# Kernel tuning notes

Measured on AMD Instinct MI355X. Metric: run time of the kernel, lower is better.

The kernel has to match this reference:

```python
import jax, jax.numpy as jnp
import numpy as np

D_MODEL = 1024
D_STATE = 16
D_CONV = 4
EXPAND = 2
D_INNER = EXPAND * D_MODEL          # 2048
DT_RANK = (D_MODEL + 15) // 16      # 64
BATCH = 2
SEQLEN = 2048


def setup_inputs() -> dict:
    key = jax.random.key(0)
    ks = jax.random.split(key, 10)

    def rn(k, shape, scale=0.02):
        return (jax.random.normal(k, shape, jnp.float32) * scale).astype(jnp.float32)

    x = jax.random.normal(ks[0], (BATCH, SEQLEN, D_MODEL), jnp.float32)
    W_in = rn(ks[1], (2 * D_INNER, D_MODEL))
    conv_w = rn(ks[2], (D_INNER, D_CONV), 0.1)
    conv_b = jnp.zeros((D_INNER,), jnp.float32)
    W_x = rn(ks[3], (DT_RANK + 2 * D_STATE, D_INNER))
    dt_std = DT_RANK ** -0.5
    W_dt = jax.random.uniform(ks[4], (D_INNER, DT_RANK), jnp.float32, -dt_std, dt_std)
    # dt bias init: inverse softplus of dt ~ LogUniform(1e-3, 1e-1)
    dt = jnp.exp(jax.random.uniform(ks[5], (D_INNER,), jnp.float32)
                 * (np.log(0.1) - np.log(0.001)) + np.log(0.001))
    dt = jnp.clip(dt, 1e-4, None)
    b_dt = dt + jnp.log(-jnp.expm1(-dt))
    # A_log = log(1..d_state) broadcast over d_inner (S4D-real init)
    A_log = jnp.log(jnp.tile(jnp.arange(1, D_STATE + 1, dtype=jnp.float32)[None, :],
                             (D_INNER, 1)))
    Dp = jnp.ones((D_INNER,), jnp.float32)
    W_out1 = rn(ks[6], (D_INNER, 2 * D_INNER))
    W_out2 = rn(ks[7], (D_MODEL, D_INNER))
    return {"x": x, "W_in": W_in, "conv_w": conv_w, "conv_b": conv_b,
            "W_x": W_x, "W_dt": W_dt, "b_dt": b_dt, "A_log": A_log,
            "Dp": Dp, "W_out1": W_out1, "W_out2": W_out2}


def _mefi_forward(x, W_in, conv_w, conv_b, W_x, W_dt, b_dt, A_log, Dp, W_out1, W_out2):
    B, L, _ = x.shape
    # in_proj: (b,l,d) -> (b, 2*d_inner, l)
    xz = jnp.einsum('bld,ed->bel', x, W_in)
    xi, z = xz[:, :D_INNER, :], xz[:, D_INNER:, :]

    # causal depthwise conv1d (left pad d_conv-1) + SiLU
    xc = jax.lax.conv_general_dilated(
        xi, conv_w[:, None, :], window_strides=(1,), padding=[(D_CONV - 1, 0)],
        dimension_numbers=('NCH', 'OIH', 'NCH'), feature_group_count=D_INNER)
    u = jax.nn.silu(xc + conv_b[None, :, None])  # (b, d_inner, l)

    # x_proj -> dt / B / C
    x_dbl = jnp.einsum('bdl,ed->ble', u, W_x)           # (b, l, dt_rank+2n)
    dt_r = x_dbl[..., :DT_RANK]                          # (b, l, r)
    Bm = x_dbl[..., DT_RANK:DT_RANK + D_STATE].transpose(0, 2, 1)  # (b, n, l)
    Cm = x_dbl[..., DT_RANK + D_STATE:].transpose(0, 2, 1)          # (b, n, l)
    dt = jnp.einsum('blr,dr->bdl', dt_r, W_dt)           # (b, d_inner, l)

    A = -jnp.exp(A_log)                                  # (d_inner, n)
    delta = jax.nn.softplus(dt + b_dt[None, :, None])    # (b, d_inner, l)

    # selective scan over time
    def step(s, inp):
        d_t, u_t, B_t, C_t = inp  # (b,d) (b,d) (b,n) (b,n)
        dA = jnp.exp(d_t[:, :, None] * A[None, :, :])
        s = dA * s + (d_t * u_t)[:, :, None] * B_t[:, None, :]
        y_t = jnp.einsum('bdn,bn->bd', s, C_t)
        return s, y_t

    s0 = jnp.zeros((B, D_INNER, D_STATE), delta.dtype)
    xs = (delta.transpose(2, 0, 1), u.transpose(2, 0, 1),
          Bm.transpose(2, 0, 1), Cm.transpose(2, 0, 1))
    _, ys = jax.lax.scan(step, s0, xs)                   # (l, b, d)
    y = ys.transpose(1, 2, 0)                            # (b, d, l)
    y = (y + Dp[None, :, None] * u) * jax.nn.silu(z)     # gated scan output

    # interaction term: tr_term = C^T @ S_t^T (S_t == A), plus D @ x
    y_t = jnp.einsum('bnl,dn->bld', Cm, A) \
        + jnp.einsum('d,bdl->bl', Dp, u)[..., None]      # (b, l, d_inner)

    # cat along channels then out_proj MLP
    y_cat = jnp.concatenate([y.transpose(0, 2, 1), y_t], axis=-1)  # (b, l, 2*d_inner)
    h = jnp.maximum(y_cat @ W_out1.T, 0.0)
    return h @ W_out2.T                                   # (b, l, d_model)


def reference(x, W_in, conv_w, conv_b, W_x, W_dt, b_dt, A_log, Dp, W_out1, W_out2):
    return _mefi_forward(x, W_in, conv_w, conv_b, W_x, W_dt, b_dt, A_log, Dp, W_out1, W_out2)
```

## Files before the change

### kernel.cpp

```cpp
#include <hip/hip_runtime.h>
#include <hip/hip_bf16.h>
#include <math.h>

#define D_MODEL 1024
#define D_STATE 16
#define D_INNER 2048
#define DT_RANK 64
#define BATCH   2
#define SEQLEN  2048
#define NPROJ   96
#define XSTR    128
#define NCHUNK  16
#define CHUNK   128
#define XKS     8

typedef __attribute__((ext_vector_type(8))) __bf16 bf16x8;
typedef __attribute__((ext_vector_type(4))) float f32x4;

__device__ __forceinline__ float silu_f(float x) { return x / (1.f + __expf(-x)); }

__device__ __forceinline__ void gload_lds16(const void* g, void* l) {
    __builtin_amdgcn_global_load_lds((const __attribute__((address_space(1))) void*)g,
                                     (__attribute__((address_space(3))) void*)l, 16, 0, 0);
}

template<int RELU, int OUT_BF16>
__global__ __launch_bounds__(256) void gemm_bf16_k(
    const __bf16* __restrict__ A, const __bf16* __restrict__ B, void* __restrict__ Cv,
    int K, int lda, int ldb, int ldc, long long sA, long long sB, long long sC)
{
    __shared__ alignas(16) __bf16 As[128 * 32];
    __shared__ alignas(16) __bf16 Bs[128 * 32];
    const int bz = blockIdx.z;
    A += (long long)bz * sA;
    B += (long long)bz * sB;
    int nwg = gridDim.x * gridDim.y;
    int flat = blockIdx.y * gridDim.x + blockIdx.x;
    int swz = (nwg & 7) ? flat : ((flat & 7) * (nwg >> 3) + (flat >> 3));
    const int m0 = (swz / gridDim.x) * 128, n0 = (swz % gridDim.x) * 128;
    const int tid = threadIdx.x;
    const int lane = tid & 63;
    const int wv = tid >> 6;
    const int wr = wv >> 1, wc = wv & 1;

    f32x4 acc[4][4];
    #pragma unroll
    for (int i = 0; i < 4; ++i)
        #pragma unroll
        for (int j = 0; j < 4; ++j) acc[i][j] = (f32x4){0.f, 0.f, 0.f, 0.f};

    const int ko = (lane >> 4) * 8;
    const int fr = lane & 15;

    for (int k0 = 0; k0 < K; k0 += 32) {
        #pragma unroll
        for (int q = 0; q < 2; ++q) {
            int f = tid + q * 256;
            int row = f >> 2, c16 = f & 3;
            gload_lds16(A + (long long)(m0 + row) * lda + k0 + c16 * 8, As + f * 8);
            gload_lds16(B + (long long)(n0 + row) * ldb + k0 + c16 * 8, Bs + f * 8);
        }
        __syncthreads();
        bf16x8 a[4], b[4];
        #pragma unroll
        for (int i = 0; i < 4; ++i) {
            a[i] = *(const bf16x8*)(As + (wr * 64 + i * 16 + fr) * 32 + ko);
            b[i] = *(const bf16x8*)(Bs + (wc * 64 + i * 16 + fr) * 32 + ko);
        }
        #pragma unroll
        for (int i = 0; i < 4; ++i)
            #pragma unroll
            for (int j = 0; j < 4; ++j)
                acc[i][j] = __builtin_amdgcn_mfma_f32_16x16x32_bf16(a[i], b[j], acc[i][j], 0, 0, 0);
        __syncthreads();
    }

    #pragma unroll
    for (int i = 0; i < 4; ++i) {
        const int row = m0 + wr * 64 + i * 16 + (lane >> 4) * 4;
        #pragma unroll
        for (int j = 0; j < 4; ++j) {
            const int col = n0 + wc * 64 + j * 16 + fr;
            #pragma unroll
            for (int r = 0; r < 4; ++r) {
                float v = acc[i][j][r];
                if (RELU) v = fmaxf(v, 0.f);
                if (OUT_BF16)
                    ((__bf16*)Cv)[(long long)bz * sC + (long long)(row + r) * ldc + col] = (__bf16)v;
                else
                    ((float*)Cv)[(long long)bz * sC + (long long)(row + r) * ldc + col] = v;
            }
        }
    }
}

__global__ void cvt_bf16_k(const float* __restrict__ in, __bf16* __restrict__ out, int n8) {
    int i = blockIdx.x * 256 + threadIdx.x;
    if (i >= n8) return;
    const f32x4* p = (const f32x4*)in + (long long)i * 2;
    f32x4 v0 = p[0], v1 = p[1];
    bf16x8 o;
    o[0] = (__bf16)v0[0]; o[1] = (__bf16)v0[1]; o[2] = (__bf16)v0[2]; o[3] = (__bf16)v0[3];
    o[4] = (__bf16)v1[0]; o[5] = (__bf16)v1[1]; o[6] = (__bf16)v1[2]; o[7] = (__bf16)v1[3];
    ((bf16x8*)out)[i] = o;
}

template<int SOFTPLUS>
__global__ __launch_bounds__(256) void gemm_nt_k(
    const float* __restrict__ A, const float* __restrict__ B, float* __restrict__ C,
    const float* __restrict__ bias,
    int M, int N, int K, int lda, int ldb, int ldc,
    long long sA, long long sB, long long sC)
{
    __shared__ float As[16][68];
    __shared__ float Bs[16][68];
    const int bz = blockIdx.z;
    A += (long long)bz * sA; B += (long long)bz * sB; C += (long long)bz * sC;
    const int m0 = blockIdx.y * 64, n0 = blockIdx.x * 64;
    const int tid = threadIdx.x;
    const int lk = tid & 15, lr = tid >> 4;
    const int tx = tid & 15, ty = tid >> 4;
    float acc[4][4] = {};
    for (int k0 = 0; k0 < K; k0 += 16) {
        #pragma unroll
        for (int q = 0; q < 4; ++q) {
            int i = lr + q * 16;
            As[lk][i] = A[(long long)(m0 + i) * lda + k0 + lk];
            Bs[lk][i] = B[(long long)(n0 + i) * ldb + k0 + lk];
        }
        __syncthreads();
        #pragma unroll
        for (int k = 0; k < 16; ++k) {
            float a[4], b[4];
            #pragma unroll
            for (int j = 0; j < 4; ++j) { a[j] = As[k][ty*4+j]; b[j] = Bs[k][tx*4+j]; }
            #pragma unroll
            for (int i = 0; i < 4; ++i)
                #pragma unroll
                for (int j = 0; j < 4; ++j) acc[i][j] += a[i] * b[j];
        }
        __syncthreads();
    }
    #pragma unroll
    for (int i = 0; i < 4; ++i) {
        const int m = m0 + ty * 4 + i;
        float bi = SOFTPLUS ? bias[m] : 0.f;
        #pragma unroll
        for (int j = 0; j < 4; ++j) {
            float v = acc[i][j];
            if (SOFTPLUS) {
                v += bi;
                v = fmaxf(v, 0.f) + log1pf(expf(-fabsf(v)));
            }
            C[(long long)m * ldc + n0 + tx*4 + j] = v;
        }
    }
}

__global__ void aneg_k(const float* __restrict__ A_log, float* __restrict__ Aneg) {
    int i = blockIdx.x * 256 + threadIdx.x;
    if (i < D_INNER * D_STATE) Aneg[i] = -expf(A_log[i]);
}

__global__ __launch_bounds__(256) void conv_silu_k(const float* __restrict__ xz,
    const float* __restrict__ cw, const float* __restrict__ cb,
    float* __restrict__ u, __bf16* __restrict__ ut)
{
    __shared__ float tile[32][33];
    const int b = blockIdx.z;
    const int d0 = blockIdx.y * 32, l0 = blockIdx.x * 32;
    const int lx = threadIdx.x, dy = threadIdx.y;
    #pragma unroll
    for (int j = 0; j < 4; ++j) {
        int d = d0 + dy + j * 8;
        const float* xi = xz + ((long long)b * 2 * D_INNER + d) * SEQLEN;
        int l = l0 + lx;
        float acc = cb[d];
        #pragma unroll
        for (int k = 0; k < 4; ++k) {
            int t = l + k - 3;
            if (t >= 0) acc += xi[t] * cw[d * 4 + k];
        }
        float v = silu_f(acc);
        u[((long long)b * D_INNER + d) * SEQLEN + l] = v;
        tile[dy + j * 8][lx] = v;
    }
    __syncthreads();
    #pragma unroll
    for (int j = 0; j < 4; ++j) {
        int l = l0 + dy + j * 8;
        ut[((long long)b * SEQLEN + l) * D_INNER + d0 + lx] = (__bf16)tile[lx][dy + j * 8];
    }
}

__global__ void xdbl_red_k(const float* __restrict__ xpart, float* __restrict__ xdbl) {
    int i = blockIdx.x * 256 + threadIdx.x;
    const f32x4* p = (const f32x4*)xpart;
    f32x4 s = p[i];
    #pragma unroll
    for (int ks = 1; ks < XKS; ++ks) {
        f32x4 v = p[(long long)ks * (BATCH * SEQLEN * XSTR / 4) + i];
        s.x += v.x; s.y += v.y; s.z += v.z; s.w += v.w;
    }
    ((f32x4*)xdbl)[i] = s;
}

__global__ __launch_bounds__(256) void scan_f_k(const float* __restrict__ delta,
    const float* __restrict__ u, const float* __restrict__ xdbl,
    const float* __restrict__ Aneg, float* __restrict__ y)
{
    __shared__ float combA[NCHUNK][16];
    __shared__ float combS[NCHUNK][16];
    __shared__ float sins[NCHUNK][16];
    __shared__ float lp[NCHUNK][16][17];
    const int tid = threadIdx.x;
    const int lane = tid & 63;
    const int n = lane & 15;
    const int c = (tid >> 6) * 4 + (lane >> 4);
    const int g = blockIdx.x;
    const int b = g >> 11, d = g & (D_INNER - 1);
    const float a = Aneg[d * D_STATE + n];
    const long long base = (long long)g * SEQLEN + c * CHUNK;
    const float4* dv = (const float4*)(delta + base);
    const float4* uv = (const float4*)(u + base);
    const float* xb = xdbl + ((long long)b * SEQLEN + c * CHUNK) * XSTR + DT_RANK + n;

    float4 pd[4], pu[4];
    float pB[16];
    #pragma unroll
    for (int i = 0; i < 4; ++i) { pd[i] = dv[i]; pu[i] = uv[i]; }
    #pragma unroll
    for (int i = 0; i < 16; ++i) pB[i] = xb[i * XSTR];

    float s = 0.f, ap = 1.f;
    for (int t0 = 0; t0 < CHUNK; t0 += 16) {
        float cd[16], cu[16], cB[16];
        #pragma unroll
        for (int i = 0; i < 4; ++i) {
            cd[4*i] = pd[i].x; cd[4*i+1] = pd[i].y; cd[4*i+2] = pd[i].z; cd[4*i+3] = pd[i].w;
            cu[4*i] = pu[i].x; cu[4*i+1] = pu[i].y; cu[4*i+2] = pu[i].z; cu[4*i+3] = pu[i].w;
        }
        #pragma unroll
        for (int i = 0; i < 16; ++i) cB[i] = pB[i];
        if (t0 + 16 < CHUNK) {
            const int nb = (t0 >> 2) + 4;
            #pragma unroll
            for (int i = 0; i < 4; ++i) { pd[i] = dv[nb + i]; pu[i] = uv[nb + i]; }
            const float* xn = xb + (t0 + 16) * XSTR;
            #pragma unroll
            for (int i = 0; i < 16; ++i) pB[i] = xn[i * XSTR];
        }
        float dA[16], wB[16];
        #pragma unroll
        for (int i = 0; i < 16; ++i) {
            dA[i] = __expf(cd[i] * a);
            wB[i] = cd[i] * cu[i] * cB[i];
        }
        #pragma unroll
        for (int i = 0; i < 16; ++i) {
            s = dA[i] * s + wB[i];
            ap *= dA[i];
        }
    }
    combA[c][n] = ap;
    combS[c][n] = s;
    __syncthreads();

    if (tid < 16) {
        float av[NCHUNK], sv[NCHUNK];
        #pragma unroll
        for (int cc = 0; cc < NCHUNK; ++cc) { av[cc] = combA[cc][tid]; sv[cc] = combS[cc][tid]; }
        float carry = 0.f;
        #pragma unroll
        for (int cc = 0; cc < NCHUNK; ++cc) {
            sins[cc][tid] = carry;
            carry = sv[cc] + av[cc] * carry;
        }
    }
    __syncthreads();

    float* yl = y + base;
    float pC[16];
    #pragma unroll
    for (int i = 0; i < 4; ++i) { pd[i] = dv[i]; pu[i] = uv[i]; }
    #pragma unroll
    for (int i = 0; i < 16; ++i) { pB[i] = xb[i * XSTR]; pC[i] = xb[i * XSTR + D_STATE]; }

    s = sins[c][n];
    for (int t0 = 0; t0 < CHUNK; t0 += 16) {
        float cd[16], cu[16], cB[16], cC[16];
        #pragma unroll
        for (int i = 0; i < 4; ++i) {
            cd[4*i] = pd[i].x; cd[4*i+1] = pd[i].y; cd[4*i+2] = pd[i].z; cd[4*i+3] = pd[i].w;
            cu[4*i] = pu[i].x; cu[4*i+1] = pu[i].y; cu[4*i+2] = pu[i].z; cu[4*i+3] = pu[i].w;
        }
        #pragma unroll
        for (int i = 0; i < 16; ++i) { cB[i] = pB[i]; cC[i] = pC[i]; }
        if (t0 + 16 < CHUNK) {
            const int nb = (t0 >> 2) + 4;
            #pragma unroll
            for (int i = 0; i < 4; ++i) { pd[i] = dv[nb + i]; pu[i] = uv[nb + i]; }
            const float* xn = xb + (t0 + 16) * XSTR;
            #pragma unroll
            for (int i = 0; i < 16; ++i) { pB[i] = xn[i * XSTR]; pC[i] = xn[i * XSTR + D_STATE]; }
        }
        float dA[16], wB[16];
        #pragma unroll
        for (int i = 0; i < 16; ++i) {
            dA[i] = __expf(cd[i] * a);
            wB[i] = cd[i] * cu[i] * cB[i];
        }
        #pragma unroll
        for (int i = 0; i < 16; ++i) {
            s = dA[i] * s + wB[i];
            lp[c][n][i] = s * cC[i];
        }
        float v[16];
        #pragma unroll
        for (int j = 0; j < 16; ++j) v[j] = lp[c][j][n];
        float acc = 0.f;
        #pragma unroll
        for (int j = 0; j < 16; ++j) acc += v[j];
        yl[t0 + n] = acc;
    }
}

__global__ void ssum_k(const float* __restrict__ u, const float* __restrict__ Dp,
                       float* __restrict__ S)
{
    int li = blockIdx.x * 256 + threadIdx.x;
    int c = blockIdx.y;
    int b = li >> 11, l = li & (SEQLEN - 1);
    const float* up = u + (long long)b * D_INNER * SEQLEN + l;
    float acc = 0.f;
    for (int d = c * 256; d < c * 256 + 256; ++d)
        acc += Dp[d] * up[(long long)d * SEQLEN];
    atomicAdd(&S[li], acc);
}

__global__ __launch_bounds__(256) void ytrans_k(const float* __restrict__ ysc,
    const float* __restrict__ u, const float* __restrict__ xz,
    const float* __restrict__ Dp, __bf16* __restrict__ ycat)
{
    __shared__ float tile[32][33];
    const int b = blockIdx.z;
    const int d0 = blockIdx.y * 32, l0 = blockIdx.x * 32;
    const int lx = threadIdx.x, dy = threadIdx.y;
    #pragma unroll
    for (int j = 0; j < 4; ++j) {
        int d = d0 + dy + j * 8;
        long long i  = ((long long)b * D_INNER + d) * SEQLEN + l0 + lx;
        long long iz = ((long long)b * 2 * D_INNER + D_INNER + d) * SEQLEN + l0 + lx;
        tile[dy + j * 8][lx] = (ysc[i] + Dp[d] * u[i]) * silu_f(xz[iz]);
    }
    __syncthreads();
    #pragma unroll
    for (int j = 0; j < 4; ++j) {
        int l = l0 + dy + j * 8;
        ycat[((long long)b * SEQLEN + l) * (2 * D_INNER) + d0 + lx] = (__bf16)tile[lx][dy + j * 8];
    }
}

__global__ __launch_bounds__(256) void yt_k(const float* __restrict__ xdbl,
    const float* __restrict__ Aneg, const float* __restrict__ S, __bf16* __restrict__ ycat)
{
    __shared__ float Cs[16][33];
    __shared__ float An[16][64];
    __shared__ float Sv[32];
    const int b = blockIdx.z;
    const int d0 = blockIdx.y * 64, l0 = blockIdx.x * 32;
    const int tid = threadIdx.x;
    for (int f = tid; f < 512; f += 256) {
        int n = f & 15, l = f >> 4;
        Cs[n][l] = xdbl[((long long)b * SEQLEN + l0 + l) * XSTR + DT_RANK + D_STATE + n];
    }
    for (int f = tid; f < 1024; f += 256) {
        int n = f & 15, d = f >> 4;
        An[n][d] = Aneg[(d0 + d) * D_STATE + n];
    }
    if (tid < 32) Sv[tid] = S[b * SEQLEN + l0 + tid];
    __syncthreads();
    const int dx = tid & 63, lg = tid >> 6;
    #pragma unroll
    for (int j = 0; j < 8; ++j) {
        int l = lg * 8 + j;
        float acc = Sv[l];
        #pragma unroll
        for (int n = 0; n < 16; ++n) acc += Cs[n][l] * An[n][dx];
        ycat[((long long)b * SEQLEN + l0 + l) * (2 * D_INNER) + D_INNER + d0 + dx] = (__bf16)acc;
    }
}

extern "C" void kernel_launch(void* const* d_in, const int* in_sizes, int n_in,
                              void* d_out, int out_size, void* d_ws, size_t ws_size,
                              hipStream_t stream)
{
    const float* x      = (const float*)d_in[0];
    const float* W_in   = (const float*)d_in[1];
    const float* conv_w = (const float*)d_in[2];
    const float* conv_b = (const float*)d_in[3];
    const float* W_x    = (const float*)d_in[4];
    const float* W_dt   = (const float*)d_in[5];
    const float* b_dt   = (const float*)d_in[6];
    const float* A_log  = (const float*)d_in[7];
    const float* Dp     = (const float*)d_in[8];
    const float* W_out1 = (const float*)d_in[9];
    const float* W_out2 = (const float*)d_in[10];
    float* out = (float*)d_out;
    float* ws  = (float*)d_ws;

    float* xz    = ws;
    float* u     = xz    + 16777216;
    float* xdblp = u     + 8388608;
    float* dtb   = xdblp + 524288;
    float* ysc   = dtb   + 8388608;
    float* Aneg  = ysc   + 8388608;
    float* S     = Aneg  + 32768;
    __bf16* ycat16 = (__bf16*)(S + 4096);
    __bf16* h16    = ycat16 + 16777216;
    __bf16* W_in16  = (__bf16*)u;
    __bf16* xb16    = W_in16 + 4194304;
    __bf16* Wout116 = (__bf16*)dtb;
    __bf16* Wout216 = Wout116 + 8388608;
    __bf16* ut16  = ycat16;
    __bf16* Wx16p = h16;
    float* xpart  = dtb;

    hipMemsetAsync(S, 0, 4096 * sizeof(float), stream);
    aneg_k<<<128, 256, 0, stream>>>(A_log, Aneg);

    cvt_bf16_k<<<2048, 256, 0, stream>>>(W_in, W_in16, 524288);
    cvt_bf16_k<<<2048, 256, 0, stream>>>(x, xb16, 524288);
    cvt_bf16_k<<<96, 256, 0, stream>>>(W_x, Wx16p, 24576);
    hipMemsetAsync(Wx16p + 96 * D_INNER, 0, 32 * D_INNER * sizeof(__bf16), stream);

    gemm_bf16_k<0, 0><<<dim3(16, 32, BATCH), 256, 0, stream>>>(
        W_in16, xb16, xz, D_MODEL, D_MODEL, D_MODEL, SEQLEN,
        0LL, (long long)SEQLEN * D_MODEL, (long long)4096 * SEQLEN);

    conv_silu_k<<<dim3(SEQLEN / 32, D_INNER / 32, BATCH), dim3(32, 8), 0, stream>>>(
        xz, conv_w, conv_b, u, ut16);

    gemm_bf16_k<0, 0><<<dim3(1, 32, XKS), 256, 0, stream>>>(
        ut16, Wx16p, xpart, D_INNER / XKS, D_INNER, D_INNER, XSTR,
        (long long)(D_INNER / XKS), (long long)(D_INNER / XKS),
        (long long)BATCH * SEQLEN * XSTR);
    xdbl_red_k<<<(BATCH * SEQLEN * XSTR / 4) / 256, 256, 0, stream>>>(xpart, xdblp);

    gemm_nt_k<1><<<dim3(SEQLEN / 64, D_INNER / 64, BATCH), 256, 0, stream>>>(
        W_dt, xdblp, dtb, b_dt, D_INNER, SEQLEN, DT_RANK, DT_RANK, XSTR, SEQLEN,
        0LL, (long long)SEQLEN * XSTR, (long long)D_INNER * SEQLEN);

    scan_f_k<<<BATCH * D_INNER, 256, 0, stream>>>(dtb, u, xdblp, Aneg, ysc);

    cvt_bf16_k<<<4096, 256, 0, stream>>>(W_out1, Wout116, 1048576);
    cvt_bf16_k<<<1024, 256, 0, stream>>>(W_out2, Wout216, 262144);

    ssum_k<<<dim3((BATCH * SEQLEN) / 256, 8), 256, 0, stream>>>(u, Dp, S);

    ytrans_k<<<dim3(SEQLEN / 32, D_INNER / 32, BATCH), dim3(32, 8), 0, stream>>>(ysc, u, xz, Dp, ycat16);

    yt_k<<<dim3(SEQLEN / 32, D_INNER / 64, BATCH), 256, 0, stream>>>(xdblp, Aneg, S, ycat16);

    gemm_bf16_k<1, 1><<<dim3(16, 32, 1), 256, 0, stream>>>(
        ycat16, Wout116, h16, 2 * D_INNER, 2 * D_INNER, 2 * D_INNER, D_INNER,
        0LL, 0LL, 0LL);

    gemm_bf16_k<0, 0><<<dim3(8, 32, 1), 256, 0, stream>>>(
        h16, Wout216, out, D_INNER, D_INNER, D_INNER, D_MODEL,
        0LL, 0LL, 0LL);
}
```

Measured before the change: 529.9 us.

## Store x_dbl transposed for coalesced scan loads and emit scan output in bf16

The x_proj GEMM now computes the transposed product, so x_dbl is stored as (feature, batch*seq). The scan kernel can then read B and C with contiguous float4 loads instead of strided scalar loads. The dt GEMM gains a transposed-B load path and yt_k is updated to match the new layout. The scan output is also written as bf16 to halve its write and read traffic, at some precision cost before the gating step.

```diff
diff --git a/kernel.cpp b/kernel.cpp
--- a/kernel.cpp
+++ b/kernel.cpp
@@ -10,6 +10,7 @@
 #define SEQLEN  2048
 #define NPROJ   96
 #define XSTR    128
+#define LFLAT   (BATCH * SEQLEN)
 #define NCHUNK  16
 #define CHUNK   128
 #define XKS     8
@@ -105,7 +106,7 @@
     ((bf16x8*)out)[i] = o;
 }
 
-template<int SOFTPLUS>
+template<int SOFTPLUS, int BT>
 __global__ __launch_bounds__(256) void gemm_nt_k(
     const float* __restrict__ A, const float* __restrict__ B, float* __restrict__ C,
     const float* __restrict__ bias,
@@ -126,7 +127,20 @@
         for (int q = 0; q < 4; ++q) {
             int i = lr + q * 16;
             As[lk][i] = A[(long long)(m0 + i) * lda + k0 + lk];
-            Bs[lk][i] = B[(long long)(n0 + i) * ldb + k0 + lk];
+        }
+        if (BT) {
+            #pragma unroll
+            for (int q = 0; q < 4; ++q) {
+                int row = (tid >> 6) + q * 4;
+                int col = tid & 63;
+                Bs[row][col] = B[(long long)(k0 + row) * ldb + n0 + col];
+            }
+        } else {
+            #pragma unroll
+            for (int q = 0; q < 4; ++q) {
+                int i = lr + q * 16;
+                Bs[lk][i] = B[(long long)(n0 + i) * ldb + k0 + lk];
+            }
         }
         __syncthreads();
         #pragma unroll
@@ -193,21 +207,21 @@
     }
 }
 
-__global__ void xdbl_red_k(const float* __restrict__ xpart, float* __restrict__ xdbl) {
+__global__ void xdbl_red_k(const float* __restrict__ xpart, float* __restrict__ xdT) {
     int i = blockIdx.x * 256 + threadIdx.x;
     const f32x4* p = (const f32x4*)xpart;
     f32x4 s = p[i];
     #pragma unroll
     for (int ks = 1; ks < XKS; ++ks) {
-        f32x4 v = p[(long long)ks * (BATCH * SEQLEN * XSTR / 4) + i];
+        f32x4 v = p[(long long)ks * (XSTR * LFLAT / 4) + i];
         s.x += v.x; s.y += v.y; s.z += v.z; s.w += v.w;
     }
-    ((f32x4*)xdbl)[i] = s;
+    ((f32x4*)xdT)[i] = s;
 }
 
 __global__ __launch_bounds__(256) void scan_f_k(const float* __restrict__ delta,
-    const float* __restrict__ u, const float* __restrict__ xdbl,
-    const float* __restrict__ Aneg, float* __restrict__ y)
+    const float* __restrict__ u, const float* __restrict__ xdT,
+    const float* __restrict__ Aneg, __bf16* __restrict__ y)
 {
     __shared__ float combA[NCHUNK][16];
     __shared__ float combS[NCHUNK][16];
@@ -223,14 +237,13 @@
     const long long base = (long long)g * SEQLEN + c * CHUNK;
     const float4* dv = (const float4*)(delta + base);
     const float4* uv = (const float4*)(u + base);
-    const float* xb = xdbl + ((long long)b * SEQLEN + c * CHUNK) * XSTR + DT_RANK + n;
-
-    float4 pd[4], pu[4];
-    float pB[16];
-    #pragma unroll
-    for (int i = 0; i < 4; ++i) { pd[i] = dv[i]; pu[i] = uv[i]; }
-    #pragma unroll
-    for (int i = 0; i < 16; ++i) pB[i] = xb[i * XSTR];
+    const long long lbase = (long long)b * SEQLEN + c * CHUNK;
+    const float4* bv = (const float4*)(xdT + (long long)(DT_RANK + n) * LFLAT + lbase);
+    const float4* cvv = (const float4*)(xdT + (long long)(DT_RANK + D_STATE + n) * LFLAT + lbase);
+
+    float4 pd[4], pu[4], pb[4];
+    #pragma unroll
+    for (int i = 0; i < 4; ++i) { pd[i] = dv[i]; pu[i] = uv[i]; pb[i] = bv[i]; }
 
     float s = 0.f, ap = 1.f;
     for (int t0 = 0; t0 < CHUNK; t0 += 16) {
@@ -239,16 +252,12 @@
         for (int i = 0; i < 4; ++i) {
             cd[4*i] = pd[i].x; cd[4*i+1] = pd[i].y; cd[4*i+2] = pd[i].z; cd[4*i+3] = pd[i].w;
             cu[4*i] = pu[i].x; cu[4*i+1] = pu[i].y; cu[4*i+2] = pu[i].z; cu[4*i+3] = pu[i].w;
-        }
-        #pragma unroll
-        for (int i = 0; i < 16; ++i) cB[i] = pB[i];
+            cB[4*i] = pb[i].x; cB[4*i+1] = pb[i].y; cB[4*i+2] = pb[i].z; cB[4*i+3] = pb[i].w;
+        }
         if (t0 + 16 < CHUNK) {
             const int nb = (t0 >> 2) + 4;
             #pragma unroll
-            for (int i = 0; i < 4; ++i) { pd[i] = dv[nb + i]; pu[i] = uv[nb + i]; }
-            const float* xn = xb + (t0 + 16) * XSTR;
-            #pragma unroll
-            for (int i = 0; i < 16; ++i) pB[i] = xn[i * XSTR];
+            for (int i = 0; i < 4; ++i) { pd[i] = dv[nb + i]; pu[i] = uv[nb + i]; pb[i] = bv[nb + i]; }
         }
         float dA[16], wB[16];
         #pragma unroll
@@ -279,12 +288,10 @@
     }
     __syncthreads();
 
-    float* yl = y + base;
-    float pC[16];
-    #pragma unroll
-    for (int i = 0; i < 4; ++i) { pd[i] = dv[i]; pu[i] = uv[i]; }
-    #pragma unroll
-    for (int i = 0; i < 16; ++i) { pB[i] = xb[i * XSTR]; pC[i] = xb[i * XSTR + D_STATE]; }
+    __bf16* yl = y + base;
+    float4 pc[4];
+    #pragma unroll
+    for (int i = 0; i < 4; ++i) { pd[i] = dv[i]; pu[i] = uv[i]; pb[i] = bv[i]; pc[i] = cvv[i]; }
 
     s = sins[c][n];
     for (int t0 = 0; t0 < CHUNK; t0 += 16) {
@@ -293,16 +300,16 @@
         for (int i = 0; i < 4; ++i) {
             cd[4*i] = pd[i].x; cd[4*i+1] = pd[i].y; cd[4*i+2] = pd[i].z; cd[4*i+3] = pd[i].w;
             cu[4*i] = pu[i].x; cu[4*i+1] = pu[i].y; cu[4*i+2] = pu[i].z; cu[4*i+3] = pu[i].w;
-        }
-        #pragma unroll
-        for (int i = 0; i < 16; ++i) { cB[i] = pB[i]; cC[i] = pC[i]; }
+            cB[4*i] = pb[i].x; cB[4*i+1] = pb[i].y; cB[4*i+2] = pb[i].z; cB[4*i+3] = pb[i].w;
+            cC[4*i] = pc[i].x; cC[4*i+1] = pc[i].y; cC[4*i+2] = pc[i].z; cC[4*i+3] = pc[i].w;
+        }
         if (t0 + 16 < CHUNK) {
             const int nb = (t0 >> 2) + 4;
             #pragma unroll
-            for (int i = 0; i < 4; ++i) { pd[i] = dv[nb + i]; pu[i] = uv[nb + i]; }
-            const float* xn = xb + (t0 + 16) * XSTR;
-            #pragma unroll
-            for (int i = 0; i < 16; ++i) { pB[i] = xn[i * XSTR]; pC[i] = xn[i * XSTR + D_STATE]; }
+            for (int i = 0; i < 4; ++i) {
+                pd[i] = dv[nb + i]; pu[i] = uv[nb + i];
+                pb[i] = bv[nb + i]; pc[i] = cvv[nb + i];
+            }
         }
         float dA[16], wB[16];
         #pragma unroll
@@ -321,7 +328,7 @@
         float acc = 0.f;
         #pragma unroll
         for (int j = 0; j < 16; ++j) acc += v[j];
-        yl[t0 + n] = acc;
+        yl[t0 + n] = (__bf16)acc;
     }
 }
 
@@ -338,7 +345,7 @@
     atomicAdd(&S[li], acc);
 }
 
-__global__ __launch_bounds__(256) void ytrans_k(const float* __restrict__ ysc,
+__global__ __launch_bounds__(256) void ytrans_k(const __bf16* __restrict__ ysc,
     const float* __restrict__ u, const float* __restrict__ xz,
     const float* __restrict__ Dp, __bf16* __restrict__ ycat)
 {
@@ -351,7 +358,7 @@
         int d = d0 + dy + j * 8;
         long long i  = ((long long)b * D_INNER + d) * SEQLEN + l0 + lx;
         long long iz = ((long long)b * 2 * D_INNER + D_INNER + d) * SEQLEN + l0 + lx;
-        tile[dy + j * 8][lx] = (ysc[i] + Dp[d] * u[i]) * silu_f(xz[iz]);
+        tile[dy + j * 8][lx] = ((float)ysc[i] + Dp[d] * u[i]) * silu_f(xz[iz]);
     }
     __syncthreads();
     #pragma unroll
@@ -361,7 +368,7 @@
     }
 }
 
-__global__ __launch_bounds__(256) void yt_k(const float* __restrict__ xdbl,
+__global__ __launch_bounds__(256) void yt_k(const float* __restrict__ xdT,
     const float* __restrict__ Aneg, const float* __restrict__ S, __bf16* __restrict__ ycat)
 {
     __shared__ float Cs[16][33];
@@ -371,8 +378,8 @@
     const int d0 = blockIdx.y * 64, l0 = blockIdx.x * 32;
     const int tid = threadIdx.x;
     for (int f = tid; f < 512; f += 256) {
-        int n = f & 15, l = f >> 4;
-        Cs[n][l] = xdbl[((long long)b * SEQLEN + l0 + l) * XSTR + DT_RANK + D_STATE + n];
+        int n = f >> 5, l = f & 31;
+        Cs[n][l] = xdT[(long long)(DT_RANK + D_STATE + n) * LFLAT + (long long)b * SEQLEN + l0 + l];
     }
     for (int f = tid; f < 1024; f += 256) {
         int n = f & 15, d = f >> 4;
@@ -411,12 +418,12 @@
 
     float* xz    = ws;
     float* u     = xz    + 16777216;
-    float* xdblp = u     + 8388608;
-    float* dtb   = xdblp + 524288;
-    float* ysc   = dtb   + 8388608;
-    float* Aneg  = ysc   + 8388608;
+    float* xdT   = u     + 8388608;
+    float* dtb   = xdT   + 524288;
+    float* Aneg  = dtb   + 8388608;
     float* S     = Aneg  + 32768;
-    __bf16* ycat16 = (__bf16*)(S + 4096);
+    __bf16* ysc16  = (__bf16*)(S + 4096);
+    __bf16* ycat16 = ysc16 + 8388608;
     __bf16* h16    = ycat16 + 16777216;
     __bf16* W_in16  = (__bf16*)u;
     __bf16* xb16    = W_in16 + 4194304;
@@ -441,26 +448,26 @@
     conv_silu_k<<<dim3(SEQLEN / 32, D_INNER / 32, BATCH), dim3(32, 8), 0, stream>>>(
         xz, conv_w, conv_b, u, ut16);
 
-    gemm_bf16_k<0, 0><<<dim3(1, 32, XKS), 256, 0, stream>>>(
-        ut16, Wx16p, xpart, D_INNER / XKS, D_INNER, D_INNER, XSTR,
+    gemm_bf16_k<0, 0><<<dim3(32, 1, XKS), 256, 0, stream>>>(
+        Wx16p, ut16, xpart, D_INNER / XKS, D_INNER, D_INNER, LFLAT,
         (long long)(D_INNER / XKS), (long long)(D_INNER / XKS),
-        (long long)BATCH * SEQLEN * XSTR);
-    xdbl_red_k<<<(BATCH * SEQLEN * XSTR / 4) / 256, 256, 0, stream>>>(xpart, xdblp);
-
-    gemm_nt_k<1><<<dim3(SEQLEN / 64, D_INNER / 64, BATCH), 256, 0, stream>>>(
-        W_dt, xdblp, dtb, b_dt, D_INNER, SEQLEN, DT_RANK, DT_RANK, XSTR, SEQLEN,
-        0LL, (long long)SEQLEN * XSTR, (long long)D_INNER * SEQLEN);
-
-    scan_f_k<<<BATCH * D_INNER, 256, 0, stream>>>(dtb, u, xdblp, Aneg, ysc);
+        (long long)XSTR * LFLAT);
+    xdbl_red_k<<<(XSTR * LFLAT / 4) / 256, 256, 0, stream>>>(xpart, xdT);
+
+    gemm_nt_k<1, 1><<<dim3(SEQLEN / 64, D_INNER / 64, BATCH), 256, 0, stream>>>(
+        W_dt, xdT, dtb, b_dt, D_INNER, SEQLEN, DT_RANK, DT_RANK, LFLAT, SEQLEN,
+        0LL, (long long)SEQLEN, (long long)D_INNER * SEQLEN);
+
+    scan_f_k<<<BATCH * D_INNER, 256, 0, stream>>>(dtb, u, xdT, Aneg, ysc16);
 
     cvt_bf16_k<<<4096, 256, 0, stream>>>(W_out1, Wout116, 1048576);
     cvt_bf16_k<<<1024, 256, 0, stream>>>(W_out2, Wout216, 262144);
 
     ssum_k<<<dim3((BATCH * SEQLEN) / 256, 8), 256, 0, stream>>>(u, Dp, S);
 
-    ytrans_k<<<dim3(SEQLEN / 32, D_INNER / 32, BATCH), dim3(32, 8), 0, stream>>>(ysc, u, xz, Dp, ycat16);
-
-    yt_k<<<dim3(SEQLEN / 32, D_INNER / 64, BATCH), 256, 0, stream>>>(xdblp, Aneg, S, ycat16);
+    ytrans_k<<<dim3(SEQLEN / 32, D_INNER / 32, BATCH), dim3(32, 8), 0, stream>>>(ysc16, u, xz, Dp, ycat16);
+
+    yt_k<<<dim3(SEQLEN / 32, D_INNER / 64, BATCH), 256, 0, stream>>>(xdT, Aneg, S, ycat16);
 
     gemm_bf16_k<1, 1><<<dim3(16, 32, 1), 256, 0, stream>>>(
         ycat16, Wout116, h16, 2 * D_INNER, 2 * D_INNER, 2 * D_INNER, D_INNER,
```

Result: slower. 620.3 us (+17.1%).
